# Performance work log

Measured on AMD Instinct MI355X. Metric: run time of the kernel, lower is better.

Reference implementation:

```python
import math
import jax, jax.numpy as jnp
import numpy as np

R = 6  # number of Hermite functions
EPS = 1e-5  # BatchNorm eps


def setup_inputs() -> dict:
    key = jax.random.key(0)
    k1, k2 = jax.random.split(key)
    B, C, H, W = 8, 64, 128, 128
    out_c = 64
    x = jax.random.normal(k1, (B, C, H, W), dtype=jnp.float32)
    gamma = jnp.ones((C,), dtype=jnp.float32)
    beta = jnp.zeros((C,), dtype=jnp.float32)
    Wt = jax.random.normal(k2, (out_c, C), dtype=jnp.float32) * (1.0 / math.sqrt(C))
    b = jnp.zeros((out_c,), dtype=jnp.float32)
    return {"x": x, "gamma": gamma, "beta": beta, "Wt": Wt, "b": b}


def _hermite_funcs(x):
    # x: (B, C, N) -> psi: (B, C, R, N)
    t = jnp.tanh(x) * math.sqrt(2 * R + 1)
    g = jnp.exp(-t * t / 2)
    pi_q = math.pi ** (-0.25)
    p_prev = pi_q * g                      # psi_0
    p_cur = math.sqrt(2.0) * pi_q * t * g  # psi_1
    ps = [p_prev, p_cur]
    for k in range(2, R):  # tiny fixed loop over recurrence order
        p_next = math.sqrt(2.0 / k) * t * p_cur - math.sqrt((k - 1) / k) * p_prev
        ps.append(p_next)
        p_prev, p_cur = p_cur, p_next
    return jnp.stack(ps, axis=2)


def reference(x, gamma, beta, Wt, b):
    B, C, H, W = x.shape
    xf = x.reshape(B, C, H * W)
    # BatchNorm1d (training-mode batch statistics, biased variance)
    mean = jnp.mean(xf, axis=(0, 2), keepdims=True)
    var = jnp.mean((xf - mean) ** 2, axis=(0, 2), keepdims=True)
    xn = (xf - mean) / jnp.sqrt(var + EPS) * gamma[None, :, None] + beta[None, :, None]
    psi = _hermite_funcs(xn)  # (B, C, R, N)
    cost = jnp.einsum('bikd,bid->bik', psi, xn)
    w = jax.nn.softmax(cost, axis=2)
    y = jnp.einsum('bik,bikd->bid', w, psi)  # (B, C, N)
    out = jnp.einsum('oc,bcd->bod', Wt, y) + b[None, :, None]  # 1x1 conv
    return out.reshape(B, Wt.shape[0], H, W)
```

## Files before the change

### kernel.cpp

```cpp
#include <hip/hip_runtime.h>

typedef short short8 __attribute__((ext_vector_type(8)));
typedef float f32x4 __attribute__((ext_vector_type(4)));

#define NB 8
#define NC 64
#define NN 16384
#define NO 64
#define SQRT13 3.605551275463989f


__device__ __forceinline__ unsigned short f2bf(float f) {
    unsigned int u = __builtin_bit_cast(unsigned int, f);
    u += 0x7fffu + ((u >> 16) & 1u);
    return (unsigned short)(u >> 16);
}

__device__ __forceinline__ unsigned int pack_bf2(float lo, float hi) {
    return (unsigned int)f2bf(lo) | ((unsigned int)f2bf(hi) << 16);
}

__device__ __forceinline__ float tanh13(float x) {
    float e = __expf(2.0f * x);
    float r = __builtin_amdgcn_rcpf(e + 1.0f);
    return fmaf(-2.0f * SQRT13, r, SQRT13);
}

__device__ __forceinline__ float yeval(float xv, float a, float bb,
                                       float c0, float c1, float c2,
                                       float c3, float c4, float c5) {
    float t = tanh13(fmaf(xv, a, bb));
    float gg = __expf(-0.5f * t * t);
    float p = c5;
    p = fmaf(p, t, c4);
    p = fmaf(p, t, c3);
    p = fmaf(p, t, c2);
    p = fmaf(p, t, c1);
    p = fmaf(p, t, c0);
    return gg * p;
}

__global__ __launch_bounds__(256) void k_stats(const float* __restrict__ x,
                                               float* __restrict__ part,
                                               const float* __restrict__ Wt,
                                               unsigned short* __restrict__ WtB) {
    int bc = blockIdx.x;
    const float* xp = x + (size_t)bc * NN;
    int tid = threadIdx.x;
    float s = 0.f, ss = 0.f;
    #pragma unroll
    for (int i = 0; i < 16; ++i) {
        float4 v = *(const float4*)(xp + i * 1024 + tid * 4);
        s  += v.x + v.y + v.z + v.w;
        ss += v.x * v.x + v.y * v.y + v.z * v.z + v.w * v.w;
    }
    for (int off = 32; off; off >>= 1) {
        s  += __shfl_down(s, off);
        ss += __shfl_down(ss, off);
    }
    __shared__ float red[2][4];
    int lane = tid & 63, wid = tid >> 6;
    if (lane == 0) { red[0][wid] = s; red[1][wid] = ss; }
    __syncthreads();
    if (tid == 0) {
        part[bc * 2 + 0] = red[0][0] + red[0][1] + red[0][2] + red[0][3];
        part[bc * 2 + 1] = red[1][0] + red[1][1] + red[1][2] + red[1][3];
    }
    if (bc == 0)
        for (int i = tid; i < 4096; i += 256) WtB[i] = f2bf(Wt[i]);
}

__global__ __launch_bounds__(512) void k_cost(const float* __restrict__ x,
                                              const float* __restrict__ part,
                                              const float* __restrict__ gamma,
                                              const float* __restrict__ beta,
                                              float* __restrict__ pp) {
    int bc = blockIdx.x;
    int c  = bc & 63;
    int tid = threadIdx.x;

    float s = 0.f, ss = 0.f;
    #pragma unroll
    for (int bb = 0; bb < NB; ++bb) {
        s  += part[(bb * NC + c) * 2 + 0];
        ss += part[(bb * NC + c) * 2 + 1];
    }
    const float inv = 1.0f / (float)(NB * NN);
    float mean = s * inv;
    float var  = ss * inv - mean * mean;
    float istd = 1.0f / sqrtf(var + 1e-5f);
    float a   = gamma[c] * istd;
    float bsh = beta[c] - mean * a;

    const float* xp = x + (size_t)bc * NN;
    float m[6] = {0.f, 0.f, 0.f, 0.f, 0.f, 0.f};

    float4 v[8];
    #pragma unroll
    for (int i = 0; i < 8; ++i)
        v[i] = *(const float4*)(xp + i * 2048 + tid * 4);
    #pragma unroll
    for (int i = 0; i < 8; ++i) {
        float xs[4] = {v[i].x, v[i].y, v[i].z, v[i].w};
        #pragma unroll
        for (int j = 0; j < 4; ++j) {
            float xn = fmaf(xs[j], a, bsh);
            float t  = tanh13(xn);
            float g  = __expf(-0.5f * t * t);
            float u  = g * xn;
            m[0] += u;
            u *= t; m[1] += u;
            u *= t; m[2] += u;
            u *= t; m[3] += u;
            u *= t; m[4] += u;
            u *= t; m[5] += u;
        }
    }

    __shared__ float red6[6][8];
    int lane = tid & 63, wid = tid >> 6;
    #pragma unroll
    for (int k = 0; k < 6; ++k) {
        float vv = m[k];
        for (int off = 32; off; off >>= 1) vv += __shfl_down(vv, off);
        if (lane == 0) red6[k][wid] = vv;
    }
    __syncthreads();
    if (tid == 0) {
        float M[6];
        #pragma unroll
        for (int k = 0; k < 6; ++k) {
            float vv = 0.f;
            #pragma unroll
            for (int w = 0; w < 8; ++w) vv += red6[k][w];
            M[k] = vv;
        }

        float h[6][6];
        #pragma unroll
        for (int k = 0; k < 6; ++k)
            #pragma unroll
            for (int j = 0; j < 6; ++j) h[k][j] = 0.f;
        h[0][0] = 0.7511255444649425f;
        h[1][1] = 1.0622519320271969f;
        for (int k = 2; k < 6; ++k) {
            float s2 = sqrtf(2.0f / k), s1 = sqrtf((k - 1.0f) / k);
            for (int j = 5; j >= 0; --j) {
                float vv = (j > 0) ? s2 * h[k - 1][j - 1] : 0.f;
                h[k][j] = vv - s1 * h[k - 2][j];
            }
        }
        float cst[6], mx = -1e30f;
        #pragma unroll
        for (int k = 0; k < 6; ++k) {
            float vv = 0.f;
            #pragma unroll
            for (int j = 0; j < 6; ++j) vv += h[k][j] * M[j];
            cst[k] = vv;
            mx = fmaxf(mx, vv);
        }
        float sum = 0.f, w[6];
        #pragma unroll
        for (int k = 0; k < 6; ++k) { w[k] = expf(cst[k] - mx); sum += w[k]; }
        float r = 1.0f / sum;
        float* P = pp + (size_t)bc * 8;
        P[0] = a; P[1] = bsh;
        #pragma unroll
        for (int j = 0; j < 6; ++j) {
            float vv = 0.f;
            #pragma unroll
            for (int k = 0; k < 6; ++k) vv += w[k] * r * h[k][j];
            P[2 + j] = vv;
        }
    }
}

__global__ __launch_bounds__(256) void k_out(const float* __restrict__ x,
                                             const unsigned short* __restrict__ WtB,
                                             const float* __restrict__ bias,
                                             const float* __restrict__ pp,
                                             float* __restrict__ out) {
    __shared__ float ppl[512];
    int tid  = threadIdx.x;
    int w    = tid >> 6;
    int l    = tid & 63;
    int grp  = l >> 4;
    int ln   = l & 15;
    int b    = blockIdx.x >> 6;
    int tile = blockIdx.x & 63;

    #pragma unroll
    for (int i0 = 0; i0 < 2; ++i0) {
        int i = i0 * 256 + tid;
        ppl[(i & 7) * 64 + (i >> 3)] = pp[(size_t)b * 512 + i];
    }
    __syncthreads();

    const float* xb = x + (size_t)b * NC * NN + tile * 256 + w * 64 + ln;

    float xr[2][4][4][2];
    #pragma unroll
    for (int kk = 0; kk < 2; ++kk)
        #pragma unroll
        for (int q = 0; q < 4; ++q) {
            int c0 = kk * 32 + grp * 8 + 2 * q;
            const float* x0 = xb + (size_t)c0 * NN;
            const float* x1 = x0 + NN;
            #pragma unroll
            for (int nd = 0; nd < 4; ++nd) {
                xr[kk][q][nd][0] = x0[nd * 16];
                xr[kk][q][nd][1] = x1[nd * 16];
            }
        }

    short8 af[2][4];
    #pragma unroll
    for (int kk = 0; kk < 2; ++kk)
        #pragma unroll
        for (int mo = 0; mo < 4; ++mo)
            af[kk][mo] = *reinterpret_cast<const short8*>(
                WtB + (mo * 16 + ln) * 64 + kk * 32 + grp * 8);

    float4 bias4[4];
    #pragma unroll
    for (int mo = 0; mo < 4; ++mo)
        bias4[mo] = *(const float4*)(bias + mo * 16 + grp * 4);

    f32x4 acc[4][4];
    #pragma unroll
    for (int mo = 0; mo < 4; ++mo)
        #pragma unroll
        for (int nd = 0; nd < 4; ++nd)
            acc[mo][nd] = (f32x4){0.f, 0.f, 0.f, 0.f};

    #pragma unroll
    for (int kk = 0; kk < 2; ++kk) {
        unsigned int bu[4][4];
        #pragma unroll
        for (int q = 0; q < 4; ++q) {
            int c0 = kk * 32 + grp * 8 + 2 * q;
            float2 A2 = *(const float2*)&ppl[c0];
            float2 B2 = *(const float2*)&ppl[64 + c0];
            float2 P0 = *(const float2*)&ppl[128 + c0];
            float2 P1 = *(const float2*)&ppl[192 + c0];
            float2 P2 = *(const float2*)&ppl[256 + c0];
            float2 P3 = *(const float2*)&ppl[320 + c0];
            float2 P4 = *(const float2*)&ppl[384 + c0];
            float2 P5 = *(const float2*)&ppl[448 + c0];
            #pragma unroll
            for (int nd = 0; nd < 4; ++nd) {
                float y0 = yeval(xr[kk][q][nd][0], A2.x, B2.x, P0.x, P1.x, P2.x, P3.x, P4.x, P5.x);
                float y1 = yeval(xr[kk][q][nd][1], A2.y, B2.y, P0.y, P1.y, P2.y, P3.y, P4.y, P5.y);
                bu[nd][q] = pack_bf2(y0, y1);
            }
        }
        #pragma unroll
        for (int nd = 0; nd < 4; ++nd) {
            union { unsigned int u[4]; short8 s; } U;
            U.u[0] = bu[nd][0]; U.u[1] = bu[nd][1];
            U.u[2] = bu[nd][2]; U.u[3] = bu[nd][3];
            #pragma unroll
            for (int mo = 0; mo < 4; ++mo)
                acc[mo][nd] = __builtin_amdgcn_mfma_f32_16x16x32_bf16(
                    af[kk][mo], U.s, acc[mo][nd], 0, 0, 0);
        }
    }

    float* ob = out + (size_t)b * NO * NN + tile * 256 + w * 64 + ln;
    #pragma unroll
    for (int mo = 0; mo < 4; ++mo) {
        #pragma unroll
        for (int nd = 0; nd < 4; ++nd) {
            f32x4 v = acc[mo][nd];
            ob[(size_t)(mo * 16 + grp * 4 + 0) * NN + nd * 16] = v[0] + bias4[mo].x;
            ob[(size_t)(mo * 16 + grp * 4 + 1) * NN + nd * 16] = v[1] + bias4[mo].y;
            ob[(size_t)(mo * 16 + grp * 4 + 2) * NN + nd * 16] = v[2] + bias4[mo].z;
            ob[(size_t)(mo * 16 + grp * 4 + 3) * NN + nd * 16] = v[3] + bias4[mo].w;
        }
    }
}

extern "C" void kernel_launch(void* const* d_in, const int* in_sizes, int n_in,
                              void* d_out, int out_size, void* d_ws, size_t ws_size,
                              hipStream_t stream) {
    const float* x     = (const float*)d_in[0];
    const float* gamma = (const float*)d_in[1];
    const float* beta  = (const float*)d_in[2];
    const float* Wt    = (const float*)d_in[3];
    const float* bias  = (const float*)d_in[4];
    float* out = (float*)d_out;
    float* ws  = (float*)d_ws;

    float* part = ws;
    float* pp   = ws + 1024;
    unsigned short* WtB = (unsigned short*)(ws + 5120);

    k_stats<<<dim3(NB * NC), dim3(256), 0, stream>>>(x, part, Wt, WtB);
    k_cost<<<dim3(NB * NC), dim3(512), 0, stream>>>(x, part, gamma, beta, pp);
    k_out<<<dim3(NB * NC), dim3(256), 0, stream>>>(x, WtB, bias, pp, out);
}
```

Measured before the change: 35.81 us.

## Fuse BatchNorm stats and cost kernels with redundant per-block channel reduction

Merges the statistics kernel and the cost kernel into one launch. Each block now recomputes the full channel mean and variance itself by reading that channel's slice from all 8 batches, with a staggered batch order. It keeps its own batch's slice in registers for the Hermite moment pass. This removes a kernel launch, the global partial-sum round trip and the second read of x. The price is roughly eight times more reads of x per block, which must be served mostly from cache to pay off.

Result: slower. 39.11 us (+9.2%).

```diff
diff --git a/kernel.cpp b/kernel.cpp
--- a/kernel.cpp
+++ b/kernel.cpp
@@ -40,68 +40,71 @@
     return gg * p;
 }
 
-__global__ __launch_bounds__(256) void k_stats(const float* __restrict__ x,
-                                               float* __restrict__ part,
-                                               const float* __restrict__ Wt,
-                                               unsigned short* __restrict__ WtB) {
+__global__ __launch_bounds__(512) void k_statcost(
+        const float* __restrict__ x, const float* __restrict__ gamma,
+        const float* __restrict__ beta, const float* __restrict__ Wt,
+        float* __restrict__ pp, unsigned short* __restrict__ WtB) {
     int bc = blockIdx.x;
-    const float* xp = x + (size_t)bc * NN;
+    int b  = bc >> 6;
+    int c  = bc & 63;
     int tid = threadIdx.x;
+    int lane = tid & 63, wid = tid >> 6;
+
+    if (bc == 0)
+        for (int i = tid; i < 4096; i += 512) WtB[i] = f2bf(Wt[i]);
+
     float s = 0.f, ss = 0.f;
-    #pragma unroll
-    for (int i = 0; i < 16; ++i) {
-        float4 v = *(const float4*)(xp + i * 1024 + tid * 4);
-        s  += v.x + v.y + v.z + v.w;
-        ss += v.x * v.x + v.y * v.y + v.z * v.z + v.w * v.w;
-    }
+
+    #pragma unroll 1
+    for (int rr = 0; rr < 7; ++rr) {
+        int bb = (b + 1 + rr) & 7;
+        const float* xp = x + ((size_t)bb * NC + c) * NN;
+        float4 v[8];
+        #pragma unroll
+        for (int i = 0; i < 8; ++i)
+            v[i] = *(const float4*)(xp + i * 2048 + tid * 4);
+        #pragma unroll
+        for (int i = 0; i < 8; ++i) {
+            s  += v[i].x + v[i].y + v[i].z + v[i].w;
+            ss += v[i].x * v[i].x + v[i].y * v[i].y + v[i].z * v[i].z + v[i].w * v[i].w;
+        }
+    }
+
+    float4 keep[8];
+    {
+        const float* xp = x + ((size_t)b * NC + c) * NN;
+        #pragma unroll
+        for (int i = 0; i < 8; ++i)
+            keep[i] = *(const float4*)(xp + i * 2048 + tid * 4);
+        #pragma unroll
+        for (int i = 0; i < 8; ++i) {
+            s  += keep[i].x + keep[i].y + keep[i].z + keep[i].w;
+            ss += keep[i].x * keep[i].x + keep[i].y * keep[i].y
+                + keep[i].z * keep[i].z + keep[i].w * keep[i].w;
+        }
+    }
+
+    __shared__ float red2[2][8];
     for (int off = 32; off; off >>= 1) {
         s  += __shfl_down(s, off);
         ss += __shfl_down(ss, off);
     }
-    __shared__ float red[2][4];
-    int lane = tid & 63, wid = tid >> 6;
-    if (lane == 0) { red[0][wid] = s; red[1][wid] = ss; }
+    if (lane == 0) { red2[0][wid] = s; red2[1][wid] = ss; }
     __syncthreads();
-    if (tid == 0) {
-        part[bc * 2 + 0] = red[0][0] + red[0][1] + red[0][2] + red[0][3];
-        part[bc * 2 + 1] = red[1][0] + red[1][1] + red[1][2] + red[1][3];
-    }
-    if (bc == 0)
-        for (int i = tid; i < 4096; i += 256) WtB[i] = f2bf(Wt[i]);
-}
-
-__global__ __launch_bounds__(512) void k_cost(const float* __restrict__ x,
-                                              const float* __restrict__ part,
-                                              const float* __restrict__ gamma,
-                                              const float* __restrict__ beta,
-                                              float* __restrict__ pp) {
-    int bc = blockIdx.x;
-    int c  = bc & 63;
-    int tid = threadIdx.x;
-
-    float s = 0.f, ss = 0.f;
-    #pragma unroll
-    for (int bb = 0; bb < NB; ++bb) {
-        s  += part[(bb * NC + c) * 2 + 0];
-        ss += part[(bb * NC + c) * 2 + 1];
-    }
+    float cs = 0.f, cq = 0.f;
+    #pragma unroll
+    for (int w2 = 0; w2 < 8; ++w2) { cs += red2[0][w2]; cq += red2[1][w2]; }
     const float inv = 1.0f / (float)(NB * NN);
-    float mean = s * inv;
-    float var  = ss * inv - mean * mean;
+    float mean = cs * inv;
+    float var  = cq * inv - mean * mean;
     float istd = 1.0f / sqrtf(var + 1e-5f);
     float a   = gamma[c] * istd;
     float bsh = beta[c] - mean * a;
 
-    const float* xp = x + (size_t)bc * NN;
     float m[6] = {0.f, 0.f, 0.f, 0.f, 0.f, 0.f};
-
-    float4 v[8];
-    #pragma unroll
-    for (int i = 0; i < 8; ++i)
-        v[i] = *(const float4*)(xp + i * 2048 + tid * 4);
     #pragma unroll
     for (int i = 0; i < 8; ++i) {
-        float xs[4] = {v[i].x, v[i].y, v[i].z, v[i].w};
+        float xs[4] = {keep[i].x, keep[i].y, keep[i].z, keep[i].w};
         #pragma unroll
         for (int j = 0; j < 4; ++j) {
             float xn = fmaf(xs[j], a, bsh);
@@ -118,7 +121,6 @@
     }
 
     __shared__ float red6[6][8];
-    int lane = tid & 63, wid = tid >> 6;
     #pragma unroll
     for (int k = 0; k < 6; ++k) {
         float vv = m[k];
@@ -132,7 +134,7 @@
         for (int k = 0; k < 6; ++k) {
             float vv = 0.f;
             #pragma unroll
-            for (int w = 0; w < 8; ++w) vv += red6[k][w];
+            for (int w2 = 0; w2 < 8; ++w2) vv += red6[k][w2];
             M[k] = vv;
         }
 
@@ -291,11 +293,9 @@
     float* out = (float*)d_out;
     float* ws  = (float*)d_ws;
 
-    float* part = ws;
-    float* pp   = ws + 1024;
-    unsigned short* WtB = (unsigned short*)(ws + 5120);
-
-    k_stats<<<dim3(NB * NC), dim3(256), 0, stream>>>(x, part, Wt, WtB);
-    k_cost<<<dim3(NB * NC), dim3(512), 0, stream>>>(x, part, gamma, beta, pp);
+    float* pp = ws;
+    unsigned short* WtB = (unsigned short*)(ws + 4096);
+
+    k_statcost<<<dim3(NB * NC), dim3(512), 0, stream>>>(x, gamma, beta, Wt, pp, WtB);
     k_out<<<dim3(NB * NC), dim3(256), 0, stream>>>(x, WtB, bias, pp, out);
 }
```
